# Kernel tuning notes

Hardware: AMD Instinct MI355X
Metric: run time of the kernel (lower is better)

## Reference

```python
import jax, jax.numpy as jnp
import numpy as np

BN_EPS = 1e-5


def setup_inputs() -> dict:
    key = jax.random.key(0)
    ks = jax.random.split(key, 8)
    B, T, D, Tu, Dout, M = 32, 4096, 128, 512, 64, 8
    feats = jax.random.normal(ks[0], (B, T, D), dtype=jnp.float32)
    # integer time-window ids stored in channel 0 of x; pin 0 and Tu-1 so
    # tw_uniq = arange(0, Tu) exactly (no -99 padding) for every batch row
    tw = jax.random.randint(ks[1], (B, T), 0, Tu)
    tw = tw.at[:, 0].set(0).at[:, 1].set(Tu - 1)
    x = jnp.concatenate([tw[..., None].astype(jnp.float32), feats], axis=-1)
    mask = jax.random.uniform(ks[2], (B, T, 1)) < 0.9
    mask = mask.at[:, :2].set(True)  # keep pinned min/max entries valid
    tw_uniq = jnp.broadcast_to(jnp.arange(Tu, dtype=jnp.float32)[None, :, None], (B, Tu, 1))
    bn_gamma = jax.random.uniform(ks[3], (D,), jnp.float32, 0.5, 1.5)
    bn_beta = 0.1 * jax.random.normal(ks[4], (D,), dtype=jnp.float32)
    bn_mean = jnp.zeros((D,), jnp.float32)
    bn_var = jnp.ones((D,), jnp.float32)
    conv_w = jax.random.normal(ks[5], (Dout, D), dtype=jnp.float32) / np.float32(np.sqrt(D))
    conv_b = jnp.zeros((Dout,), jnp.float32)
    fc_w = jax.random.normal(ks[6], (M, Dout), dtype=jnp.float32) / np.float32(np.sqrt(Dout))
    fc_b = jnp.zeros((M,), jnp.float32)
    return dict(x=x, mask=mask, tw_uniq=tw_uniq, bn_gamma=bn_gamma, bn_beta=bn_beta,
                bn_mean=bn_mean, bn_var=bn_var, conv_w=conv_w, conv_b=conv_b,
                fc_w=fc_w, fc_b=fc_b)


def reference(x, mask, tw_uniq, bn_gamma, bn_beta, bn_mean, bn_var,
              conv_w, conv_b, fc_w, fc_b):
    # --- TimeWindowPooling (segment-max form of the dense expand+where+amax) ---
    # torch computes amax_T(where(tw==tw_uniq & mask, x, 0)) -> max(0, group max).
    # Equivalent: scatter-max of mask-zeroed values into a zeros-initialized
    # (B, Tu, D) buffer, avoiding the O(B*T*Tu*D) blowup.
    tw = x[..., 0]           # (B, T) integer-valued, detached in torch
    feats = x[..., 1:]       # (B, T, D)
    B, T, D = feats.shape
    Tu = tw_uniq.shape[1]
    u0 = tw_uniq[:, 0, 0]    # per-batch window minimum
    idx = jnp.clip((tw - u0[:, None]).astype(jnp.int32), 0, Tu - 1)  # (B, T)
    vals = jnp.where(mask, feats, 0.0)  # masked rows contribute 0 == init value
    hidden = jnp.zeros((B, Tu, D), feats.dtype).at[jnp.arange(B)[:, None], idx].max(vals)
    # --- mlp_down: BatchNorm1d (inference stats) + 1x1 Conv1d over channels ---
    h = (hidden - bn_mean) * jax.lax.rsqrt(bn_var + BN_EPS) * bn_gamma + bn_beta
    h = jnp.einsum('bud,od->buo', h, conv_w) + conv_b  # (B, Tu, Dout)
    # --- fc_out ---
    return jnp.einsum('buo,mo->bum', h, fc_w) + fc_b   # (B, Tu, M)
```

## Files before the change

### kernel.cpp

```cpp
#include <hip/hip_runtime.h>

#define B_   32
#define T_   4096
#define D_   128
#define TU   512
#define M_   8
#define O_   64
#define DCH  16
#define NCH  8
#define PAD  17
#define BN_EPS 1e-5f
#define UB   8

__global__ __launch_bounds__(1024) void fused_scatter_mm_kernel(
    const float* __restrict__ x,
    const int*   __restrict__ mask,
    const float* __restrict__ tw_uniq,
    const float* __restrict__ bn_gamma,
    const float* __restrict__ bn_beta,
    const float* __restrict__ bn_mean,
    const float* __restrict__ bn_var,
    const float* __restrict__ conv_w,
    const float* __restrict__ conv_b,
    const float* __restrict__ fc_w,
    const float* __restrict__ fc_b,
    float*       __restrict__ out) {
    __shared__ unsigned hid[TU * PAD];
    __shared__ float wsm[M_ * DCH];
    __shared__ float tmp[M_ * DCH];
    __shared__ float biasc[M_];
    const int i = blockIdx.x;
    const int b = (i & 7) + 8 * ((i >> 3) & 3);
    const int c = i >> 5;
    const int tid = threadIdx.x;

    for (int p = tid; p < TU * PAD; p += 1024) hid[p] = 0u;
    if (tid < M_ * DCH) {
        const int m = tid >> 4, dl = tid & (DCH - 1), d = c * DCH + dl;
        float wraw = 0.f;
#pragma unroll
        for (int o = 0; o < O_; ++o) wraw += fc_w[m * O_ + o] * conv_w[o * D_ + d];
        const float sc = bn_gamma[d] * rsqrtf(bn_var[d] + BN_EPS);
        const float sh = bn_beta[d] - bn_mean[d] * sc;
        wsm[tid] = wraw * sc;
        tmp[tid] = wraw * sh;
    }
    __syncthreads();
    if (tid < M_) {
        float s = 0.f;
#pragma unroll
        for (int d = 0; d < DCH; ++d) s += tmp[tid * DCH + d];
        if (c == 0) {
            s += fc_b[tid];
            for (int o = 0; o < O_; ++o) s += fc_w[tid * O_ + o] * conv_b[o];
        }
        biasc[tid] = s;
    }

    const float* xb = x + (size_t)b * T_ * (D_ + 1);
    const int*   mb = mask + b * T_;
    const float  u0 = tw_uniq[b * TU];

    const int dl = tid & (DCH - 1);
    const int g  = tid >> 4;
    for (int it = 0; it < T_ / 64 / UB; ++it) {
        float fv[UB], twf[UB];
        int   mk[UB];
#pragma unroll
        for (int j = 0; j < UB; ++j) {
            const int t = (it * UB + j) * 64 + g;
            const float* row = xb + (size_t)t * (D_ + 1);
            fv[j]  = row[1 + c * DCH + dl];
            twf[j] = row[0];
            mk[j]  = mb[t];
        }
#pragma unroll
        for (int j = 0; j < UB; ++j) {
            if (mk[j] != 0 && fv[j] > 0.0f) {
                int u = (int)(twf[j] - u0);
                u = min(max(u, 0), TU - 1);
                atomicMax(&hid[u * PAD + dl], __float_as_uint(fv[j]));
            }
        }
    }
    __syncthreads();

    const int u  = tid & (TU - 1);
    const int mh = tid >> 9;
    float a0 = biasc[mh * 4 + 0];
    float a1 = biasc[mh * 4 + 1];
    float a2 = biasc[mh * 4 + 2];
    float a3 = biasc[mh * 4 + 3];
#pragma unroll
    for (int d = 0; d < DCH; ++d) {
        float h = __uint_as_float(hid[u * PAD + d]);
        a0 += h * wsm[(mh * 4 + 0) * DCH + d];
        a1 += h * wsm[(mh * 4 + 1) * DCH + d];
        a2 += h * wsm[(mh * 4 + 2) * DCH + d];
        a3 += h * wsm[(mh * 4 + 3) * DCH + d];
    }
    float* op = out + ((size_t)(b * TU + u)) * M_ + mh * 4;
    atomicAdd(op + 0, a0);
    atomicAdd(op + 1, a1);
    atomicAdd(op + 2, a2);
    atomicAdd(op + 3, a3);
}

extern "C" void kernel_launch(void* const* d_in, const int* in_sizes, int n_in,
                              void* d_out, int out_size, void* d_ws, size_t ws_size,
                              hipStream_t stream) {
    const float* x        = (const float*)d_in[0];
    const int*   mask     = (const int*)  d_in[1];
    const float* tw_uniq  = (const float*)d_in[2];
    const float* bn_gamma = (const float*)d_in[3];
    const float* bn_beta  = (const float*)d_in[4];
    const float* bn_mean  = (const float*)d_in[5];
    const float* bn_var   = (const float*)d_in[6];
    const float* conv_w   = (const float*)d_in[7];
    const float* conv_b   = (const float*)d_in[8];
    const float* fc_w     = (const float*)d_in[9];
    const float* fc_b     = (const float*)d_in[10];
    float* out = (float*)d_out;

    hipMemsetAsync(out, 0, (size_t)out_size * sizeof(float), stream);
    fused_scatter_mm_kernel<<<256, 1024, 0, stream>>>(
        x, mask, tw_uniq, bn_gamma, bn_beta, bn_mean, bn_var,
        conv_w, conv_b, fc_w, fc_b, out);
}
```

Before: 144.3 us.

## Vectorize feature loads and replace output atomics with workspace reduction

Each thread now loads four consecutive feature channels per row through an unaligned 4-wide vector load, so one thread covers four channels and four lanes cover a channel chunk. The per-row mask and time-window index are then computed once per four channels instead of once per channel. The global atomicAdd accumulation across channel-chunk blocks and the output memset are replaced by per-chunk partial writes to a workspace, summed by a second reduce kernel. This adds a kernel launch and extra workspace traffic, and the unaligned vector loads on the 129-float row stride may split into several memory transactions.

```diff
diff --git a/kernel.cpp b/kernel.cpp
--- a/kernel.cpp
+++ b/kernel.cpp
@@ -10,7 +10,11 @@
 #define NCH  8
 #define PAD  17
 #define BN_EPS 1e-5f
-#define UB   8
+#define UB   4
+
+typedef float f4u __attribute__((ext_vector_type(4), aligned(4)));
+
+#define WS_STRIDE (B_ * TU * M_)
 
 __global__ __launch_bounds__(1024) void fused_scatter_mm_kernel(
     const float* __restrict__ x,
@@ -24,7 +28,7 @@
     const float* __restrict__ conv_b,
     const float* __restrict__ fc_w,
     const float* __restrict__ fc_b,
-    float*       __restrict__ out) {
+    float*       __restrict__ ws) {
     __shared__ unsigned hid[TU * PAD];
     __shared__ float wsm[M_ * DCH];
     __shared__ float tmp[M_ * DCH];
@@ -61,25 +65,29 @@
     const int*   mb = mask + b * T_;
     const float  u0 = tw_uniq[b * TU];
 
-    const int dl = tid & (DCH - 1);
-    const int g  = tid >> 4;
-    for (int it = 0; it < T_ / 64 / UB; ++it) {
-        float fv[UB], twf[UB];
+    const int q = tid & 3;
+    const int r = tid >> 2;
+    for (int it = 0; it < T_ / 256 / UB; ++it) {
+        f4u   fv[UB];
+        float twf[UB];
         int   mk[UB];
 #pragma unroll
         for (int j = 0; j < UB; ++j) {
-            const int t = (it * UB + j) * 64 + g;
+            const int t = (it * UB + j) * 256 + r;
             const float* row = xb + (size_t)t * (D_ + 1);
-            fv[j]  = row[1 + c * DCH + dl];
+            fv[j]  = *(const f4u*)(row + 1 + c * DCH + q * 4);
             twf[j] = row[0];
             mk[j]  = mb[t];
         }
 #pragma unroll
         for (int j = 0; j < UB; ++j) {
-            if (mk[j] != 0 && fv[j] > 0.0f) {
-                int u = (int)(twf[j] - u0);
-                u = min(max(u, 0), TU - 1);
-                atomicMax(&hid[u * PAD + dl], __float_as_uint(fv[j]));
+            if (mk[j] != 0) {
+                int u = min(max((int)(twf[j] - u0), 0), TU - 1);
+                unsigned* hp = &hid[u * PAD + q * 4];
+                if (fv[j].x > 0.0f) atomicMax(hp + 0, __float_as_uint(fv[j].x));
+                if (fv[j].y > 0.0f) atomicMax(hp + 1, __float_as_uint(fv[j].y));
+                if (fv[j].z > 0.0f) atomicMax(hp + 2, __float_as_uint(fv[j].z));
+                if (fv[j].w > 0.0f) atomicMax(hp + 3, __float_as_uint(fv[j].w));
             }
         }
     }
@@ -99,11 +107,22 @@
         a2 += h * wsm[(mh * 4 + 2) * DCH + d];
         a3 += h * wsm[(mh * 4 + 3) * DCH + d];
     }
-    float* op = out + ((size_t)(b * TU + u)) * M_ + mh * 4;
-    atomicAdd(op + 0, a0);
-    atomicAdd(op + 1, a1);
-    atomicAdd(op + 2, a2);
-    atomicAdd(op + 3, a3);
+    float4 av = make_float4(a0, a1, a2, a3);
+    float* wp = ws + (size_t)c * WS_STRIDE + ((size_t)(b * TU + u)) * M_ + mh * 4;
+    *(float4*)wp = av;
+}
+
+__global__ __launch_bounds__(256) void reduce_kernel(
+    const float* __restrict__ ws, float* __restrict__ out) {
+    const int j = blockIdx.x;
+    const int s = j >> 3;
+    const int b = (j & 7) + 8 * (s & 3);
+    const int uc = s >> 2;
+    const int idx = (b * TU + uc * 32) * M_ + threadIdx.x;
+    float acc = 0.f;
+#pragma unroll
+    for (int c = 0; c < NCH; ++c) acc += ws[(size_t)c * WS_STRIDE + idx];
+    out[idx] = acc;
 }
 
 extern "C" void kernel_launch(void* const* d_in, const int* in_sizes, int n_in,
@@ -120,10 +139,11 @@
     const float* conv_b   = (const float*)d_in[8];
     const float* fc_w     = (const float*)d_in[9];
     const float* fc_b     = (const float*)d_in[10];
+    float* ws  = (float*)d_ws;
     float* out = (float*)d_out;
 
-    hipMemsetAsync(out, 0, (size_t)out_size * sizeof(float), stream);
     fused_scatter_mm_kernel<<<256, 1024, 0, stream>>>(
         x, mask, tw_uniq, bn_gamma, bn_beta, bn_mean, bn_var,
-        conv_w, conv_b, fc_w, fc_b, out);
+        conv_w, conv_b, fc_w, fc_b, ws);
+    reduce_kernel<<<512, 256, 0, stream>>>(ws, out);
 }
```

Result: faster. 128.8 us (-10.8%).
